# Kernel optimization log

Measured on AMD Instinct MI355X. Metric: run time of the kernel, lower is better.

## Reference

```python
import jax, jax.numpy as jnp
import numpy as np

EMB_DIM = 1024
HEAD = 16
HEAD_DIM = EMB_DIM // HEAD


def setup_inputs() -> dict:
    key = jax.random.key(0)
    ks = jax.random.split(key, 6)
    s = 1.0 / np.sqrt(EMB_DIM)
    return {
        "z": jax.random.normal(ks[0], (4, 2048, EMB_DIM), dtype=jnp.float32),
        "w_q": jax.random.normal(ks[1], (EMB_DIM, EMB_DIM), dtype=jnp.float32) * s,
        "w_k": jax.random.normal(ks[2], (EMB_DIM, EMB_DIM), dtype=jnp.float32) * s,
        "w_v": jax.random.normal(ks[3], (EMB_DIM, EMB_DIM), dtype=jnp.float32) * s,
        "w_o": jax.random.normal(ks[4], (EMB_DIM, EMB_DIM), dtype=jnp.float32) * s,
        "b_o": jax.random.normal(ks[5], (EMB_DIM,), dtype=jnp.float32) * 0.01,
    }


def reference(z, w_q, w_k, w_v, w_o, b_o):
    B, N, D = z.shape
    # QKV projections (nn.Linear: x @ W.T; here weights stored as (D_in, D_out))
    q = (z @ w_q).reshape(B, N, HEAD, HEAD_DIM).transpose(0, 2, 1, 3)  # bhnd
    k = (z @ w_k).reshape(B, N, HEAD, HEAD_DIM).transpose(0, 2, 1, 3)
    v = (z @ w_v).reshape(B, N, HEAD, HEAD_DIM).transpose(0, 2, 1, 3)
    scale = 1.0 / np.sqrt(HEAD_DIM).astype(np.float32)
    dots = jnp.einsum("bhnd,bhmd->bhnm", q, k) * scale
    attn = jax.nn.softmax(dots, axis=-1)
    out = jnp.einsum("bhnm,bhmd->bhnd", attn, v)
    out = out.transpose(0, 2, 1, 3).reshape(B, N, D)
    return out @ w_o + b_o
```

## Files before the change

### kernel.cpp

```cpp
#include <hip/hip_runtime.h>
#include <hip/hip_bf16.h>
#include <stdint.h>

typedef unsigned short u16;
typedef __attribute__((ext_vector_type(8))) short bf16x8;
typedef __attribute__((ext_vector_type(4))) float f32x4;
typedef __attribute__((ext_vector_type(16))) float f32x16;

static __device__ inline u16 f2bf(float f) {
  union { float f; uint32_t u; } v; v.f = f;
  uint32_t u = v.u;
  u += 0x7fffu + ((u >> 16) & 1);
  return (u16)(u >> 16);
}

static __device__ inline float fast_exp2(float x) {
#if __has_builtin(__builtin_amdgcn_exp2f)
  return __builtin_amdgcn_exp2f(x);
#else
  return __expf(x * 0.6931471805599453f);
#endif
}

static __device__ inline uint32_t pack_bf16(float lo, float hi) {
#if __has_builtin(__builtin_amdgcn_cvt_pk_bf16_f32)
  typedef __attribute__((ext_vector_type(2))) __bf16 bf16x2_t;
  bf16x2_t r = __builtin_amdgcn_cvt_pk_bf16_f32(lo, hi);
  union { bf16x2_t v; uint32_t u; } c; c.v = r;
  return c.u;
#else
  union { float f; uint32_t u; } a, b;
  a.f = lo; b.f = hi;
  uint32_t ua = a.u + 0x8000u;
  uint32_t ub = b.u + 0x8000u;
  return __builtin_amdgcn_perm(ub, ua, 0x07060302u);
#endif
}

static __device__ __forceinline__ void load_lds_128(const u16* g, u16* l) {
  __builtin_amdgcn_global_load_lds((const __attribute__((address_space(1))) void*)g,
                                   (__attribute__((address_space(3))) void*)l,
                                   16, 0, 0);
}

__global__ __launch_bounds__(256) void cast_bf16_kernel(const float* __restrict__ src,
                                                        u16* __restrict__ dst, int n4) {
  int i = blockIdx.x * 256 + threadIdx.x;
  if (i < n4) {
    float4 v = reinterpret_cast<const float4*>(src)[i];
    uint2 o;
    o.x = pack_bf16(v.x, v.y);
    o.y = pack_bf16(v.z, v.w);
    reinterpret_cast<uint2*>(dst)[i] = o;
  }
}

__global__ __launch_bounds__(256) void wtrans_kernel(const float* __restrict__ wq,
                                                     const float* __restrict__ wk,
                                                     const float* __restrict__ wv,
                                                     const float* __restrict__ wo,
                                                     u16* __restrict__ bqkv,
                                                     u16* __restrict__ wot) {
  int z = blockIdx.z;
  const float* src = (z == 0) ? wq : (z == 1) ? wk : (z == 2) ? wv : wo;
  u16* dst = (z < 3) ? (bqkv + (size_t)z * 1024 * 1024) : wot;
  __shared__ float tile[32][33];
  int c0 = blockIdx.x * 32, r0 = blockIdx.y * 32;
  int tx = threadIdx.x, ty = threadIdx.y;
#pragma unroll
  for (int i = 0; i < 32; i += 8)
    tile[ty + i][tx] = src[(size_t)(r0 + ty + i) * 1024 + c0 + tx];
  __syncthreads();
#pragma unroll
  for (int i = 0; i < 32; i += 8)
    dst[(size_t)(c0 + ty + i) * 1024 + r0 + tx] = f2bf(tile[tx][ty + i]);
}

template <int MODE>
__global__ __launch_bounds__(256) void gemm_bt_kernel(
    const u16* __restrict__ A, const u16* __restrict__ Bt,
    u16* __restrict__ outQ, u16* __restrict__ outK, u16* __restrict__ outVt,
    float* __restrict__ outC, const float* __restrict__ bias) {
  const int Kd = 1024;
  const int n0 = blockIdx.x * 128;
  const int m0 = blockIdx.y * 128;
  __shared__ __align__(16) u16 Asm[128 * 32];
  __shared__ __align__(16) u16 Bsm[128 * 32];
  const int tid = threadIdx.x;
  const int wave = tid >> 6, lane = tid & 63;
  const int quad = lane >> 4, l15 = lane & 15;
  const int wm = (wave >> 1) * 64, wn = (wave & 1) * 64;

  const int c0 = wave * 128 + lane;
  const int c1 = c0 + 64;
  const int r0 = c0 >> 2, p0 = (c0 & 3) * 8;
  const int r1 = c1 >> 2, p1 = (c1 & 3) * 8;

  const u16* Ab = A + (size_t)m0 * Kd;
  const u16* Bb = Bt + (size_t)n0 * Kd;

  f32x4 acc[4][4] = {};

  for (int k0 = 0; k0 < Kd; k0 += 32) {
    __syncthreads();
    load_lds_128(Ab + (size_t)r0 * Kd + k0 + p0, Asm + c0 * 8);
    load_lds_128(Ab + (size_t)r1 * Kd + k0 + p1, Asm + c1 * 8);
    load_lds_128(Bb + (size_t)r0 * Kd + k0 + p0, Bsm + c0 * 8);
    load_lds_128(Bb + (size_t)r1 * Kd + k0 + p1, Bsm + c1 * 8);
    __syncthreads();
    bf16x8 af[4], bf[4];
#pragma unroll
    for (int i = 0; i < 4; i++)
      af[i] = *reinterpret_cast<const bf16x8*>(Asm + (wm + i * 16 + l15) * 32 + quad * 8);
#pragma unroll
    for (int i = 0; i < 4; i++)
      bf[i] = *reinterpret_cast<const bf16x8*>(Bsm + (wn + i * 16 + l15) * 32 + quad * 8);
#pragma unroll
    for (int mi = 0; mi < 4; mi++)
#pragma unroll
      for (int ni = 0; ni < 4; ni++)
        acc[mi][ni] = __builtin_amdgcn_mfma_f32_16x16x32_bf16(af[mi], bf[ni], acc[mi][ni], 0, 0, 0);
  }

  if (MODE == 0) {
    const int which = (n0 + wn) >> 10;
#pragma unroll
    for (int mi = 0; mi < 4; mi++)
#pragma unroll
      for (int ni = 0; ni < 4; ni++) {
        int n = n0 + wn + ni * 16 + l15;
        int hn = n & 1023;
        int h = hn >> 6, dim = hn & 63;
        if (which == 2) {
          int m = m0 + wm + mi * 16 + quad * 4;
          int b = m >> 11, tok = m & 2047;
          uint2 pk;
          pk.x = pack_bf16(acc[mi][ni][0], acc[mi][ni][1]);
          pk.y = pack_bf16(acc[mi][ni][2], acc[mi][ni][3]);
          *reinterpret_cast<uint2*>(outVt + ((size_t)(b * 16 + h) * 64 + dim) * 2048 + tok) = pk;
        } else {
          u16* dst = (which == 0) ? outQ : outK;
          float qscale = (which == 0) ? 0.1803368801111204f : 1.0f;
#pragma unroll
          for (int r = 0; r < 4; r++) {
            int m = m0 + wm + mi * 16 + quad * 4 + r;
            int b = m >> 11, tok = m & 2047;
            dst[(((size_t)(b * 16 + h)) * 2048 + tok) * 64 + dim] = f2bf(acc[mi][ni][r] * qscale);
          }
        }
      }
  } else {
#pragma unroll
    for (int mi = 0; mi < 4; mi++)
#pragma unroll
      for (int ni = 0; ni < 4; ni++) {
        int n = n0 + wn + ni * 16 + l15;
        float bv = bias[n];
#pragma unroll
        for (int r = 0; r < 4; r++) {
          int m = m0 + wm + mi * 16 + quad * 4 + r;
          outC[(size_t)m * 1024 + n] = acc[mi][ni][r] + bv;
        }
      }
  }
}

__global__ __launch_bounds__(256, 3) void attn_kernel(const u16* __restrict__ Q,
                                                      const u16* __restrict__ K,
                                                      const u16* __restrict__ Vt,
                                                      u16* __restrict__ Oout) {
  const int bh = blockIdx.x;
  const int q0 = blockIdx.y * 128;
  const int tid = threadIdx.x;
  const int wave = tid >> 6, lane = tid & 63;
  const int l31 = lane & 31, h = lane >> 5;
  const int e = l31 & 7;

  __shared__ __align__(16) u16 Kb2[2][4096];
  __shared__ __align__(16) u16 Vb2[2][4096];

  const u16* Qg = Q + ((size_t)bh * 2048 + q0 + wave * 32) * 64;
  const u16* Kg = K + (size_t)bh * 2048 * 64;
  const u16* Vg = Vt + (size_t)bh * 64 * 2048;

  bf16x8 qf[4];
#pragma unroll
  for (int dc = 0; dc < 4; dc++)
    qf[dc] = *reinterpret_cast<const bf16x8*>(Qg + (size_t)l31 * 64 + dc * 16 + h * 8);

  const int s0 = tid, s1 = tid + 256;
  const int sr0 = s0 >> 3, sg0 = ((s0 & 7) ^ (sr0 & 7)) * 8;
  const int sr1 = s1 >> 3, sg1 = ((s1 & 7) ^ (sr1 & 7)) * 8;

  load_lds_128(Kg + (size_t)sr0 * 64 + sg0, &Kb2[0][s0 * 8]);
  load_lds_128(Kg + (size_t)sr1 * 64 + sg1, &Kb2[0][s1 * 8]);
  load_lds_128(Vg + (size_t)sr0 * 2048 + sg0, &Vb2[0][s0 * 8]);
  load_lds_128(Vg + (size_t)sr1 * 2048 + sg1, &Vb2[0][s1 * 8]);
  __syncthreads();

  float ls0 = 0.f, ls1 = 0.f;
  f32x16 oacc[2] = {};
  int cur = 0;

  for (int kt = 0; kt < 2048; kt += 64) {
    const u16* uK = &Kb2[cur][0];
    const u16* uV = &Vb2[cur][0];

    bf16x8 kfr[2][4], vfr[2][2][2];
#pragma unroll
    for (int kb = 0; kb < 2; kb++)
#pragma unroll
      for (int dc = 0; dc < 4; dc++)
        kfr[kb][dc] = *reinterpret_cast<const bf16x8*>(
            uK + (kb * 32 + l31) * 64 + (((2 * dc + h) ^ e) * 8));
#pragma unroll
    for (int dt = 0; dt < 2; dt++)
#pragma unroll
      for (int kb = 0; kb < 2; kb++)
#pragma unroll
        for (int kc = 0; kc < 2; kc++)
          vfr[dt][kb][kc] = *reinterpret_cast<const bf16x8*>(
              uV + (dt * 32 + l31) * 64 + (((4 * kb + 2 * kc + h) ^ e) * 8));

    if (kt + 64 < 2048) {
      const int nb = cur ^ 1;
      load_lds_128(Kg + (size_t)(kt + 64 + sr0) * 64 + sg0, &Kb2[nb][s0 * 8]);
      load_lds_128(Kg + (size_t)(kt + 64 + sr1) * 64 + sg1, &Kb2[nb][s1 * 8]);
      load_lds_128(Vg + (size_t)sr0 * 2048 + kt + 64 + sg0, &Vb2[nb][s0 * 8]);
      load_lds_128(Vg + (size_t)sr1 * 2048 + kt + 64 + sg1, &Vb2[nb][s1 * 8]);
    }

#pragma unroll
    for (int kb = 0; kb < 2; kb++) {
      f32x16 s = {};
#pragma unroll
      for (int dc = 0; dc < 4; dc++)
        s = __builtin_amdgcn_mfma_f32_32x32x16_bf16(kfr[kb][dc], qf[dc], s, 0, 0, 0);
      float p[16];
#pragma unroll
      for (int i = 0; i < 16; i++) p[i] = fast_exp2(s[i]);
#pragma unroll
      for (int i = 0; i < 16; i += 2) { ls0 += p[i]; ls1 += p[i + 1]; }
      uint2 pk[4];
#pragma unroll
      for (int rq = 0; rq < 4; rq++) {
        pk[rq].x = pack_bf16(p[rq * 4 + 0], p[rq * 4 + 1]);
        pk[rq].y = pack_bf16(p[rq * 4 + 2], p[rq * 4 + 3]);
      }
      uint2 snd0 = h ? pk[0] : pk[1];
      uint2 snd1 = h ? pk[2] : pk[3];
      uint2 rx0, rx1;
      rx0.x = __shfl_xor((int)snd0.x, 32, 64); rx0.y = __shfl_xor((int)snd0.y, 32, 64);
      rx1.x = __shfl_xor((int)snd1.x, 32, 64); rx1.y = __shfl_xor((int)snd1.y, 32, 64);
      uint4 b0, b1;
      b0.x = h ? rx0.x : pk[0].x;  b0.y = h ? rx0.y : pk[0].y;
      b0.z = h ? pk[1].x : rx0.x;  b0.w = h ? pk[1].y : rx0.y;
      b1.x = h ? rx1.x : pk[2].x;  b1.y = h ? rx1.y : pk[2].y;
      b1.z = h ? pk[3].x : rx1.x;  b1.w = h ? pk[3].y : rx1.y;
      union { uint4 u; bf16x8 v; } bf0, bf1;
      bf0.u = b0; bf1.u = b1;
#pragma unroll
      for (int dt = 0; dt < 2; dt++) {
        oacc[dt] = __builtin_amdgcn_mfma_f32_32x32x16_bf16(vfr[dt][kb][0], bf0.v, oacc[dt], 0, 0, 0);
        oacc[dt] = __builtin_amdgcn_mfma_f32_32x32x16_bf16(vfr[dt][kb][1], bf1.v, oacc[dt], 0, 0, 0);
      }
    }

    __syncthreads();
    cur ^= 1;
  }

  float lsum = ls0 + ls1;
  lsum += __shfl_xor(lsum, 32, 64);
  float inv = __builtin_amdgcn_rcpf(lsum);

  const int b = bh >> 4, hd = bh & 15;
  u16* dst = Oout + (size_t)b * 2048 * 1024 + (size_t)hd * 64;
  const size_t qrow = (size_t)(q0 + wave * 32 + l31) * 1024;
#pragma unroll
  for (int dt = 0; dt < 2; dt++)
#pragma unroll
    for (int rq = 0; rq < 4; rq++) {
      uint2 o;
      o.x = pack_bf16(oacc[dt][rq * 4 + 0] * inv, oacc[dt][rq * 4 + 1] * inv);
      o.y = pack_bf16(oacc[dt][rq * 4 + 2] * inv, oacc[dt][rq * 4 + 3] * inv);
      *reinterpret_cast<uint2*>(dst + qrow + dt * 32 + rq * 8 + h * 4) = o;
    }
}

extern "C" void kernel_launch(void* const* d_in, const int* in_sizes, int n_in,
                              void* d_out, int out_size, void* d_ws, size_t ws_size,
                              hipStream_t stream) {
  (void)in_sizes; (void)n_in; (void)out_size; (void)ws_size;
  const float* z  = (const float*)d_in[0];
  const float* wq = (const float*)d_in[1];
  const float* wk = (const float*)d_in[2];
  const float* wv = (const float*)d_in[3];
  const float* wo = (const float*)d_in[4];
  const float* bo = (const float*)d_in[5];
  float* out = (float*)d_out;

  char* ws = (char*)d_ws;
  u16* zb   = (u16*)(ws);
  u16* bqkv = (u16*)(ws + (16ull << 20));
  u16* wot  = (u16*)(ws + (22ull << 20));
  u16* Qb   = (u16*)(ws + (24ull << 20));
  u16* Kb   = (u16*)(ws + (40ull << 20));
  u16* Vtb  = (u16*)(ws + (56ull << 20));
  u16* Ob   = zb;

  cast_bf16_kernel<<<8192, 256, 0, stream>>>(z, zb, 2097152);
  wtrans_kernel<<<dim3(32, 32, 4), dim3(32, 8), 0, stream>>>(wq, wk, wv, wo, bqkv, wot);
  gemm_bt_kernel<0><<<dim3(24, 64), 256, 0, stream>>>(zb, bqkv, Qb, Kb, Vtb, nullptr, nullptr);
  attn_kernel<<<dim3(64, 16), 256, 0, stream>>>(Qb, Kb, Vtb, Ob);
  gemm_bt_kernel<1><<<dim3(8, 64), 256, 0, stream>>>(Ob, wot, nullptr, nullptr, nullptr, out, bo);
}
```

Before: 295.8 us.

## Process two 32-row query tiles per wave in attention and use permlane32 swap

Each wave in the attention kernel now handles 64 query rows (two 32-row sub-tiles) instead of 32. K/V fragments loaded from LDS are reused across both sub-tiles, and the grid shrinks to half as many blocks with launch bounds lowered to 2 blocks per CU. The shuffle-and-select exchange of P fragments between wave halves is replaced by the permlane32_swap builtin when available. This costs more registers per thread (double accumulators and Q fragments) and gives fewer blocks for the GPU to schedule.

```diff
diff --git a/kernel.cpp b/kernel.cpp
--- a/kernel.cpp
+++ b/kernel.cpp
@@ -34,6 +34,20 @@
   uint32_t ua = a.u + 0x8000u;
   uint32_t ub = b.u + 0x8000u;
   return __builtin_amdgcn_perm(ub, ua, 0x07060302u);
+#endif
+}
+
+static __device__ __forceinline__ void plswap(uint32_t a, uint32_t b,
+                                              uint32_t& x, uint32_t& y) {
+#if __has_builtin(__builtin_amdgcn_permlane32_swap)
+  auto r = __builtin_amdgcn_permlane32_swap(a, b, false, false);
+  x = (uint32_t)r[0]; y = (uint32_t)r[1];
+#else
+  int h = (threadIdx.x & 63) >> 5;
+  uint32_t pa = (uint32_t)__shfl_xor((int)a, 32, 64);
+  uint32_t pb = (uint32_t)__shfl_xor((int)b, 32, 64);
+  x = h ? pb : a;
+  y = h ? b : pa;
 #endif
 }
 
@@ -165,12 +179,12 @@
   }
 }
 
-__global__ __launch_bounds__(256, 3) void attn_kernel(const u16* __restrict__ Q,
+__global__ __launch_bounds__(256, 2) void attn_kernel(const u16* __restrict__ Q,
                                                       const u16* __restrict__ K,
                                                       const u16* __restrict__ Vt,
                                                       u16* __restrict__ Oout) {
   const int bh = blockIdx.x;
-  const int q0 = blockIdx.y * 128;
+  const int q0 = blockIdx.y * 256;
   const int tid = threadIdx.x;
   const int wave = tid >> 6, lane = tid & 63;
   const int l31 = lane & 31, h = lane >> 5;
@@ -179,14 +193,17 @@
   __shared__ __align__(16) u16 Kb2[2][4096];
   __shared__ __align__(16) u16 Vb2[2][4096];
 
-  const u16* Qg = Q + ((size_t)bh * 2048 + q0 + wave * 32) * 64;
+  const u16* Qg = Q + ((size_t)bh * 2048 + q0 + wave * 64) * 64;
   const u16* Kg = K + (size_t)bh * 2048 * 64;
   const u16* Vg = Vt + (size_t)bh * 64 * 2048;
 
-  bf16x8 qf[4];
-#pragma unroll
-  for (int dc = 0; dc < 4; dc++)
-    qf[dc] = *reinterpret_cast<const bf16x8*>(Qg + (size_t)l31 * 64 + dc * 16 + h * 8);
+  bf16x8 qf[2][4];
+#pragma unroll
+  for (int j = 0; j < 2; j++)
+#pragma unroll
+    for (int dc = 0; dc < 4; dc++)
+      qf[j][dc] = *reinterpret_cast<const bf16x8*>(
+          Qg + (size_t)(j * 32 + l31) * 64 + dc * 16 + h * 8);
 
   const int s0 = tid, s1 = tid + 256;
   const int sr0 = s0 >> 3, sg0 = ((s0 & 7) ^ (sr0 & 7)) * 8;
@@ -198,8 +215,8 @@
   load_lds_128(Vg + (size_t)sr1 * 2048 + sg1, &Vb2[0][s1 * 8]);
   __syncthreads();
 
-  float ls0 = 0.f, ls1 = 0.f;
-  f32x16 oacc[2] = {};
+  float ls[2][2] = {};
+  f32x16 oacc[2][2] = {};
   int cur = 0;
 
   for (int kt = 0; kt < 2048; kt += 64) {
@@ -231,61 +248,60 @@
     }
 
 #pragma unroll
-    for (int kb = 0; kb < 2; kb++) {
-      f32x16 s = {};
-#pragma unroll
-      for (int dc = 0; dc < 4; dc++)
-        s = __builtin_amdgcn_mfma_f32_32x32x16_bf16(kfr[kb][dc], qf[dc], s, 0, 0, 0);
-      float p[16];
-#pragma unroll
-      for (int i = 0; i < 16; i++) p[i] = fast_exp2(s[i]);
-#pragma unroll
-      for (int i = 0; i < 16; i += 2) { ls0 += p[i]; ls1 += p[i + 1]; }
-      uint2 pk[4];
-#pragma unroll
-      for (int rq = 0; rq < 4; rq++) {
-        pk[rq].x = pack_bf16(p[rq * 4 + 0], p[rq * 4 + 1]);
-        pk[rq].y = pack_bf16(p[rq * 4 + 2], p[rq * 4 + 3]);
+    for (int kb = 0; kb < 2; kb++)
+#pragma unroll
+      for (int j = 0; j < 2; j++) {
+        f32x16 s = {};
+#pragma unroll
+        for (int dc = 0; dc < 4; dc++)
+          s = __builtin_amdgcn_mfma_f32_32x32x16_bf16(kfr[kb][dc], qf[j][dc], s, 0, 0, 0);
+        float p[16];
+#pragma unroll
+        for (int i = 0; i < 16; i++) p[i] = fast_exp2(s[i]);
+#pragma unroll
+        for (int i = 0; i < 16; i += 2) { ls[j][0] += p[i]; ls[j][1] += p[i + 1]; }
+        uint32_t pk[4][2];
+#pragma unroll
+        for (int rq = 0; rq < 4; rq++) {
+          pk[rq][0] = pack_bf16(p[rq * 4 + 0], p[rq * 4 + 1]);
+          pk[rq][1] = pack_bf16(p[rq * 4 + 2], p[rq * 4 + 3]);
+        }
+        uint4 b0, b1;
+        plswap(pk[0][0], pk[1][0], b0.x, b0.z);
+        plswap(pk[0][1], pk[1][1], b0.y, b0.w);
+        plswap(pk[2][0], pk[3][0], b1.x, b1.z);
+        plswap(pk[2][1], pk[3][1], b1.y, b1.w);
+        union { uint4 u; bf16x8 v; } bf0, bf1;
+        bf0.u = b0; bf1.u = b1;
+#pragma unroll
+        for (int dt = 0; dt < 2; dt++) {
+          oacc[j][dt] = __builtin_amdgcn_mfma_f32_32x32x16_bf16(vfr[dt][kb][0], bf0.v, oacc[j][dt], 0, 0, 0);
+          oacc[j][dt] = __builtin_amdgcn_mfma_f32_32x32x16_bf16(vfr[dt][kb][1], bf1.v, oacc[j][dt], 0, 0, 0);
+        }
       }
-      uint2 snd0 = h ? pk[0] : pk[1];
-      uint2 snd1 = h ? pk[2] : pk[3];
-      uint2 rx0, rx1;
-      rx0.x = __shfl_xor((int)snd0.x, 32, 64); rx0.y = __shfl_xor((int)snd0.y, 32, 64);
-      rx1.x = __shfl_xor((int)snd1.x, 32, 64); rx1.y = __shfl_xor((int)snd1.y, 32, 64);
-      uint4 b0, b1;
-      b0.x = h ? rx0.x : pk[0].x;  b0.y = h ? rx0.y : pk[0].y;
-      b0.z = h ? pk[1].x : rx0.x;  b0.w = h ? pk[1].y : rx0.y;
-      b1.x = h ? rx1.x : pk[2].x;  b1.y = h ? rx1.y : pk[2].y;
-      b1.z = h ? pk[3].x : rx1.x;  b1.w = h ? pk[3].y : rx1.y;
-      union { uint4 u; bf16x8 v; } bf0, bf1;
-      bf0.u = b0; bf1.u = b1;
-#pragma unroll
-      for (int dt = 0; dt < 2; dt++) {
-        oacc[dt] = __builtin_amdgcn_mfma_f32_32x32x16_bf16(vfr[dt][kb][0], bf0.v, oacc[dt], 0, 0, 0);
-        oacc[dt] = __builtin_amdgcn_mfma_f32_32x32x16_bf16(vfr[dt][kb][1], bf1.v, oacc[dt], 0, 0, 0);
-      }
-    }
 
     __syncthreads();
     cur ^= 1;
   }
 
-  float lsum = ls0 + ls1;
-  lsum += __shfl_xor(lsum, 32, 64);
-  float inv = __builtin_amdgcn_rcpf(lsum);
-
   const int b = bh >> 4, hd = bh & 15;
   u16* dst = Oout + (size_t)b * 2048 * 1024 + (size_t)hd * 64;
-  const size_t qrow = (size_t)(q0 + wave * 32 + l31) * 1024;
-#pragma unroll
-  for (int dt = 0; dt < 2; dt++)
-#pragma unroll
-    for (int rq = 0; rq < 4; rq++) {
-      uint2 o;
-      o.x = pack_bf16(oacc[dt][rq * 4 + 0] * inv, oacc[dt][rq * 4 + 1] * inv);
-      o.y = pack_bf16(oacc[dt][rq * 4 + 2] * inv, oacc[dt][rq * 4 + 3] * inv);
-      *reinterpret_cast<uint2*>(dst + qrow + dt * 32 + rq * 8 + h * 4) = o;
-    }
+#pragma unroll
+  for (int j = 0; j < 2; j++) {
+    float lsum = ls[j][0] + ls[j][1];
+    lsum += __shfl_xor(lsum, 32, 64);
+    float inv = __builtin_amdgcn_rcpf(lsum);
+    const size_t qrow = (size_t)(q0 + wave * 64 + j * 32 + l31) * 1024;
+#pragma unroll
+    for (int dt = 0; dt < 2; dt++)
+#pragma unroll
+      for (int rq = 0; rq < 4; rq++) {
+        uint2 o;
+        o.x = pack_bf16(oacc[j][dt][rq * 4 + 0] * inv, oacc[j][dt][rq * 4 + 1] * inv);
+        o.y = pack_bf16(oacc[j][dt][rq * 4 + 2] * inv, oacc[j][dt][rq * 4 + 3] * inv);
+        *reinterpret_cast<uint2*>(dst + qrow + dt * 32 + rq * 8 + h * 4) = o;
+      }
+  }
 }
 
 extern "C" void kernel_launch(void* const* d_in, const int* in_sizes, int n_in,
@@ -312,6 +328,6 @@
   cast_bf16_kernel<<<8192, 256, 0, stream>>>(z, zb, 2097152);
   wtrans_kernel<<<dim3(32, 32, 4), dim3(32, 8), 0, stream>>>(wq, wk, wv, wo, bqkv, wot);
   gemm_bt_kernel<0><<<dim3(24, 64), 256, 0, stream>>>(zb, bqkv, Qb, Kb, Vtb, nullptr, nullptr);
-  attn_kernel<<<dim3(64, 16), 256, 0, stream>>>(Qb, Kb, Vtb, Ob);
+  attn_kernel<<<dim3(64, 8), 256, 0, stream>>>(Qb, Kb, Vtb, Ob);
   gemm_bt_kernel<1><<<dim3(8, 64), 256, 0, stream>>>(Ob, wot, nullptr, nullptr, nullptr, out, bo);
 }
```

Result: faster. 281.8 us (-4.7%).
